# Performance work log

Measured on AMD Instinct MI355X. Metric: run time of the kernel, lower is better.

The kernel has to match this reference:

```python
import jax, jax.numpy as jnp
import numpy as np

N_NODES = 50000
BN_EPS = 1e-5


def gcn_conv(x, W, b, src, dst, n):
    # PyG GCNConv: add self-loops, symmetric normalization, linear then scatter-add, bias after.
    h = x @ W                                             # [N, out]
    loops = jnp.arange(n, dtype=src.dtype)
    s = jnp.concatenate([src, loops])                     # [E+N]
    d = jnp.concatenate([dst, loops])                     # [E+N]
    deg = jax.ops.segment_sum(jnp.ones_like(d, dtype=h.dtype), d, num_segments=n)
    dinv = jnp.where(deg > 0, jax.lax.rsqrt(deg), 0.0)    # deg^-1/2
    norm = dinv[s] * dinv[d]                              # [E+N]
    msg = h[s] * norm[:, None]                            # gather + scale
    out = jax.ops.segment_sum(msg, d, num_segments=n)     # scatter-add to targets
    return out + b


def batch_norm(x, gamma, beta):
    # training-mode BatchNorm1d: batch stats over node dim, biased variance
    mean = jnp.mean(x, axis=0)
    var = jnp.mean(jnp.square(x - mean), axis=0)
    return (x - mean) * jax.lax.rsqrt(var + BN_EPS) * gamma + beta


def setup_inputs() -> dict:
    key = jax.random.key(0)
    ks = jax.random.split(key, 4)
    n, e = N_NODES, 800000
    c_in, c_hid, c_out = 128, 128, 64
    x = jax.random.normal(ks[0], (n, c_in), dtype=jnp.float32)
    edge_index = jax.random.randint(ks[1], (2, e), 0, n, dtype=jnp.int64)
    W1 = jax.random.normal(ks[2], (c_in, c_hid), dtype=jnp.float32) / np.sqrt(c_in)
    W2 = jax.random.normal(ks[3], (c_hid, c_out), dtype=jnp.float32) / np.sqrt(c_hid)
    return {
        "x": x,
        "edge_index": edge_index,
        "W1": W1,
        "b1": jnp.zeros((c_hid,), jnp.float32),
        "gamma": jnp.ones((c_hid,), jnp.float32),
        "beta": jnp.zeros((c_hid,), jnp.float32),
        "W2": W2,
        "b2": jnp.zeros((c_out,), jnp.float32),
    }


def reference(x, edge_index, W1, b1, gamma, beta, W2, b2):
    src, dst = edge_index[0], edge_index[1]
    n = x.shape[0]
    h = gcn_conv(x, W1, b1, src, dst, n)
    h = batch_norm(h, gamma, beta)
    h = jax.nn.elu(h)
    z = gcn_conv(h, W2, b2, src, dst, n)
    return z
```

## Files before the change

### kernel.cpp

```cpp
#include <hip/hip_runtime.h>
#include <math.h>

#define C_IN 128
#define C_HID 128
#define C_OUT 64
#define BN_EPS 1e-5f
#define CHUNK 1024
#define NBB 96
#define CAP 108192

typedef unsigned int uint;
typedef int iv4 __attribute__((ext_vector_type(4)));

__device__ __forceinline__ void fma4(float4& a, float s, const float4& b) {
    a.x += s * b.x; a.y += s * b.y; a.z += s * b.z; a.w += s * b.w;
}
__device__ __forceinline__ uint bfr(float f) {
    uint u = __float_as_uint(f);
    return (u + 0x7fffu + ((u >> 16) & 1u)) >> 16;
}
__device__ __forceinline__ uint pk(float a, float b) { return bfr(a) | (bfr(b) << 16); }
__device__ __forceinline__ float bl(uint u) { return __uint_as_float(u << 16); }
__device__ __forceinline__ float bh(uint u) { return __uint_as_float(u & 0xffff0000u); }

__global__ __launch_bounds__(256) void k_zero(int* __restrict__ deg,
                                              float* __restrict__ gsum,
                                              float* __restrict__ gss,
                                              int* __restrict__ bcur, int n) {
    int i = blockIdx.x * 256 + threadIdx.x;
    if (i < n) deg[i] = 0;
    else if (i < n + 128) gsum[i - n] = 0.f;
    else if (i < n + 256) gss[i - n - 128] = 0.f;
    else if (i < n + 264) bcur[i - n - 256] = 0;
}

__global__ __launch_bounds__(256) void k_bucket(const int* __restrict__ src,
                                                const int* __restrict__ dst,
                                                int* __restrict__ deg,
                                                int* __restrict__ bcur,
                                                int2* __restrict__ stage,
                                                int E, float binv) {
    __shared__ int cnt[8], base[8], off[8];
    if (threadIdx.x < 8) { cnt[threadIdx.x] = 0; off[threadIdx.x] = 0; }
    __syncthreads();
    int e0 = blockIdx.x * CHUNK;
    int e1 = e0 + CHUNK; if (e1 > E) e1 = E;
    int nv = (e1 - e0) & ~3;
    for (int e = e0 + threadIdx.x * 4; e < e0 + nv; e += 1024) {
        iv4 d4 = *(const iv4*)&dst[e];
        #pragma unroll
        for (int j = 0; j < 4; ++j) {
            int d = d4[j];
            atomicAdd(&deg[d], 1);
            int b = (int)((float)d * binv); if (b > 7) b = 7;
            atomicAdd(&cnt[b], 1);
        }
    }
    for (int e = e0 + nv + threadIdx.x; e < e1; e += 256) {
        int d = dst[e];
        atomicAdd(&deg[d], 1);
        int b = (int)((float)d * binv); if (b > 7) b = 7;
        atomicAdd(&cnt[b], 1);
    }
    __syncthreads();
    if (threadIdx.x < 8) base[threadIdx.x] = atomicAdd(&bcur[threadIdx.x], cnt[threadIdx.x]);
    __syncthreads();
    for (int e = e0 + threadIdx.x * 4; e < e0 + nv; e += 1024) {
        iv4 d4 = *(const iv4*)&dst[e];
        iv4 s4 = *(const iv4*)&src[e];
        #pragma unroll
        for (int j = 0; j < 4; ++j) {
            int d = d4[j], s = s4[j];
            int b = (int)((float)d * binv); if (b > 7) b = 7;
            int o = base[b] + atomicAdd(&off[b], 1);
            if (o < CAP) stage[(size_t)b * CAP + o] = make_int2(d, s);
        }
    }
    for (int e = e0 + nv + threadIdx.x; e < e1; e += 256) {
        int d = dst[e], s = src[e];
        int b = (int)((float)d * binv); if (b > 7) b = 7;
        int o = base[b] + atomicAdd(&off[b], 1);
        if (o < CAP) stage[(size_t)b * CAP + o] = make_int2(d, s);
    }
}

__global__ __launch_bounds__(256) void k_part(const int* __restrict__ deg,
                                              int* __restrict__ part, int n) {
    int i = blockIdx.x * 256 + threadIdx.x;
    int v = (i < n) ? deg[i] : 0;
    #pragma unroll
    for (int o = 32; o > 0; o >>= 1) v += __shfl_down(v, o);
    __shared__ int ls[4];
    if ((threadIdx.x & 63) == 0) ls[threadIdx.x >> 6] = v;
    __syncthreads();
    if (threadIdx.x == 0) part[blockIdx.x] = ls[0] + ls[1] + ls[2] + ls[3];
}

__global__ __launch_bounds__(256) void k_scanp(int* __restrict__ part, int nb) {
    __shared__ int s[256];
    int tid = threadIdx.x;
    int v = (tid < nb) ? part[tid] : 0;
    s[tid] = v;
    __syncthreads();
    for (int o = 1; o < 256; o <<= 1) {
        int t = (tid >= o) ? s[tid - o] : 0;
        __syncthreads();
        s[tid] += t;
        __syncthreads();
    }
    if (tid < nb) part[tid] = s[tid] - v;
}

__global__ __launch_bounds__(256) void k_apply(const int* __restrict__ deg,
                                               const int* __restrict__ part,
                                               int* __restrict__ rowstart,
                                               int* __restrict__ cursor,
                                               float* __restrict__ dinv, int n) {
    int i = blockIdx.x * 256 + threadIdx.x;
    int d = (i < n) ? deg[i] : 0;
    __shared__ int s[256];
    s[threadIdx.x] = d;
    __syncthreads();
    for (int o = 1; o < 256; o <<= 1) {
        int t = (threadIdx.x >= o) ? s[threadIdx.x - o] : 0;
        __syncthreads();
        s[threadIdx.x] += t;
        __syncthreads();
    }
    int incl = s[threadIdx.x];
    int off = part[blockIdx.x];
    if (i < n) {
        rowstart[i] = off + incl - d;
        cursor[i]   = off + incl - d;
        dinv[i] = rsqrtf((float)(d + 1));
        if (i == n - 1) rowstart[n] = off + incl;
    }
}

__global__ __launch_bounds__(256) void k_fill2(const int2* __restrict__ stage,
                                               const int* __restrict__ bcur,
                                               int* __restrict__ cursor,
                                               int* __restrict__ csr) {
    int b = blockIdx.x & 7;
    int j = blockIdx.x >> 3;
    int cnt = bcur[b]; if (cnt > CAP) cnt = CAP;
    const int2* sp = stage + (size_t)b * CAP;
    for (int i = j * 256 + threadIdx.x; i < cnt; i += NBB * 256) {
        int2 pr = sp[i];
        csr[atomicAdd(&cursor[pr.x], 1)] = pr.y;
    }
}

__global__ __launch_bounds__(256) void k_gemm1(const float* __restrict__ x,
                                               const float* __restrict__ W,
                                               uint* __restrict__ h, int n) {
    __shared__ float xs[64][68];
    __shared__ float ws[64][68];
    const int tid = threadIdx.x;
    const int cg = tid & 15, rg = tid >> 4;
    const int c0 = cg * 4, r0 = rg * 4;
    const int base = blockIdx.x * 64;
    const int ccol = blockIdx.y * 64;

    float4 acc0 = make_float4(0.f, 0.f, 0.f, 0.f);
    float4 acc1 = acc0, acc2 = acc0, acc3 = acc0;

    for (int p = 0; p < 2; ++p) {
        const int k0 = p * 64;
        if (p) __syncthreads();
        for (int idx = tid; idx < 64 * 16; idx += 256) {
            int row = idx >> 4, c4 = (idx & 15) * 4;
            float4 v = make_float4(0.f, 0.f, 0.f, 0.f);
            if (base + row < n) v = *(const float4*)&x[(size_t)(base + row) * C_IN + k0 + c4];
            *(float4*)&xs[row][c4] = v;
        }
        for (int idx = tid; idx < 64 * 16; idx += 256) {
            int kk = idx >> 4, cc = (idx & 15) * 4;
            *(float4*)&ws[kk][cc] = *(const float4*)&W[(size_t)(k0 + kk) * C_HID + ccol + cc];
        }
        __syncthreads();
        for (int kk = 0; kk < 64; kk += 4) {
            float4 xv0 = *(const float4*)&xs[r0 + 0][kk];
            float4 xv1 = *(const float4*)&xs[r0 + 1][kk];
            float4 xv2 = *(const float4*)&xs[r0 + 2][kk];
            float4 xv3 = *(const float4*)&xs[r0 + 3][kk];
            float4 wv0 = *(const float4*)&ws[kk + 0][c0];
            float4 wv1 = *(const float4*)&ws[kk + 1][c0];
            float4 wv2 = *(const float4*)&ws[kk + 2][c0];
            float4 wv3 = *(const float4*)&ws[kk + 3][c0];
            fma4(acc0, xv0.x, wv0); fma4(acc0, xv0.y, wv1); fma4(acc0, xv0.z, wv2); fma4(acc0, xv0.w, wv3);
            fma4(acc1, xv1.x, wv0); fma4(acc1, xv1.y, wv1); fma4(acc1, xv1.z, wv2); fma4(acc1, xv1.w, wv3);
            fma4(acc2, xv2.x, wv0); fma4(acc2, xv2.y, wv1); fma4(acc2, xv2.z, wv2); fma4(acc2, xv2.w, wv3);
            fma4(acc3, xv3.x, wv0); fma4(acc3, xv3.y, wv1); fma4(acc3, xv3.z, wv2); fma4(acc3, xv3.w, wv3);
        }
    }
    const int cu = (ccol + c0) >> 1;
    if (base + r0 + 0 < n) { uint2 o = make_uint2(pk(acc0.x, acc0.y), pk(acc0.z, acc0.w)); *(uint2*)&h[(size_t)(base + r0 + 0) * 64 + cu] = o; }
    if (base + r0 + 1 < n) { uint2 o = make_uint2(pk(acc1.x, acc1.y), pk(acc1.z, acc1.w)); *(uint2*)&h[(size_t)(base + r0 + 1) * 64 + cu] = o; }
    if (base + r0 + 2 < n) { uint2 o = make_uint2(pk(acc2.x, acc2.y), pk(acc2.z, acc2.w)); *(uint2*)&h[(size_t)(base + r0 + 2) * 64 + cu] = o; }
    if (base + r0 + 3 < n) { uint2 o = make_uint2(pk(acc3.x, acc3.y), pk(acc3.z, acc3.w)); *(uint2*)&h[(size_t)(base + r0 + 3) * 64 + cu] = o; }
}

__global__ __launch_bounds__(256) void k_gather1(const uint4* __restrict__ h,
                                                 const float* __restrict__ dinv,
                                                 const int* __restrict__ rowstart,
                                                 const int* __restrict__ csr,
                                                 const float* __restrict__ b,
                                                 uint4* __restrict__ g1, int n) {
    int v = (blockIdx.x * 256 + threadIdx.x) >> 4;
    int l = threadIdx.x & 15;
    if (v >= n) return;
    float dv = dinv[v];
    int s0 = rowstart[v], s1 = rowstart[v + 1];
    float4 aA, aB;
    {
        uint4 u = h[(size_t)v * 16 + l];
        aA.x = dv * bl(u.x); aA.y = dv * bh(u.x); aA.z = dv * bl(u.y); aA.w = dv * bh(u.y);
        aB.x = dv * bl(u.z); aB.y = dv * bh(u.z); aB.z = dv * bl(u.w); aB.w = dv * bh(u.w);
    }
    int e = s0;
    for (; e + 3 < s1; e += 4) {
        int i0 = csr[e], i1 = csr[e + 1], i2 = csr[e + 2], i3 = csr[e + 3];
        float w0 = dinv[i0], w1 = dinv[i1], w2 = dinv[i2], w3 = dinv[i3];
        uint4 u0 = h[(size_t)i0 * 16 + l];
        uint4 u1 = h[(size_t)i1 * 16 + l];
        uint4 u2 = h[(size_t)i2 * 16 + l];
        uint4 u3 = h[(size_t)i3 * 16 + l];
        aA.x += w0 * bl(u0.x) + w1 * bl(u1.x) + w2 * bl(u2.x) + w3 * bl(u3.x);
        aA.y += w0 * bh(u0.x) + w1 * bh(u1.x) + w2 * bh(u2.x) + w3 * bh(u3.x);
        aA.z += w0 * bl(u0.y) + w1 * bl(u1.y) + w2 * bl(u2.y) + w3 * bl(u3.y);
        aA.w += w0 * bh(u0.y) + w1 * bh(u1.y) + w2 * bh(u2.y) + w3 * bh(u3.y);
        aB.x += w0 * bl(u0.z) + w1 * bl(u1.z) + w2 * bl(u2.z) + w3 * bl(u3.z);
        aB.y += w0 * bh(u0.z) + w1 * bh(u1.z) + w2 * bh(u2.z) + w3 * bh(u3.z);
        aB.z += w0 * bl(u0.w) + w1 * bl(u1.w) + w2 * bl(u2.w) + w3 * bl(u3.w);
        aB.w += w0 * bh(u0.w) + w1 * bh(u1.w) + w2 * bh(u2.w) + w3 * bh(u3.w);
    }
    for (; e < s1; ++e) {
        int s = csr[e];
        float w = dinv[s];
        uint4 u = h[(size_t)s * 16 + l];
        aA.x += w * bl(u.x); aA.y += w * bh(u.x); aA.z += w * bl(u.y); aA.w += w * bh(u.y);
        aB.x += w * bl(u.z); aB.y += w * bh(u.z); aB.z += w * bl(u.w); aB.w += w * bh(u.w);
    }
    float4 b0 = *(const float4*)&b[l * 8];
    float4 b1v = *(const float4*)&b[l * 8 + 4];
    uint4 o;
    o.x = pk(aA.x * dv + b0.x,  aA.y * dv + b0.y);
    o.y = pk(aA.z * dv + b0.z,  aA.w * dv + b0.w);
    o.z = pk(aB.x * dv + b1v.x, aB.y * dv + b1v.y);
    o.w = pk(aB.z * dv + b1v.z, aB.w * dv + b1v.w);
    g1[(size_t)v * 16 + l] = o;
}

__global__ __launch_bounds__(256) void k_bnstats(const uint4* __restrict__ g,
                                                 float* __restrict__ gsum,
                                                 float* __restrict__ gss, int n) {
    float4 sA = make_float4(0.f,0.f,0.f,0.f), sB = sA, qA = sA, qB = sA;
    int total = n * 16;
    int stride = gridDim.x * 256;
    for (int i = blockIdx.x * 256 + threadIdx.x; i < total; i += stride) {
        uint4 u = g[i];
        float v0 = bl(u.x), v1 = bh(u.x), v2 = bl(u.y), v3 = bh(u.y);
        float v4 = bl(u.z), v5 = bh(u.z), v6 = bl(u.w), v7 = bh(u.w);
        sA.x += v0; sA.y += v1; sA.z += v2; sA.w += v3;
        sB.x += v4; sB.y += v5; sB.z += v6; sB.w += v7;
        qA.x += v0*v0; qA.y += v1*v1; qA.z += v2*v2; qA.w += v3*v3;
        qB.x += v4*v4; qB.y += v5*v5; qB.z += v6*v6; qB.w += v7*v7;
    }
    __shared__ float sb[128], qb[128];
    if (threadIdx.x < 128) { sb[threadIdx.x] = 0.f; qb[threadIdx.x] = 0.f; }
    __syncthreads();
    int c0 = (threadIdx.x & 15) * 8;
    atomicAdd(&sb[c0+0], sA.x); atomicAdd(&sb[c0+1], sA.y); atomicAdd(&sb[c0+2], sA.z); atomicAdd(&sb[c0+3], sA.w);
    atomicAdd(&sb[c0+4], sB.x); atomicAdd(&sb[c0+5], sB.y); atomicAdd(&sb[c0+6], sB.z); atomicAdd(&sb[c0+7], sB.w);
    atomicAdd(&qb[c0+0], qA.x); atomicAdd(&qb[c0+1], qA.y); atomicAdd(&qb[c0+2], qA.z); atomicAdd(&qb[c0+3], qA.w);
    atomicAdd(&qb[c0+4], qB.x); atomicAdd(&qb[c0+5], qB.y); atomicAdd(&qb[c0+6], qB.z); atomicAdd(&qb[c0+7], qB.w);
    __syncthreads();
    if (threadIdx.x < 128) {
        atomicAdd(&gsum[threadIdx.x], sb[threadIdx.x]);
        atomicAdd(&gss[threadIdx.x], qb[threadIdx.x]);
    }
}

__global__ __launch_bounds__(256) void k_gemm2(const uint4* __restrict__ g1,
                                               const float* __restrict__ W2,
                                               const float* __restrict__ gsum,
                                               const float* __restrict__ gss,
                                               const float* __restrict__ gamma,
                                               const float* __restrict__ beta,
                                               uint* __restrict__ h2, int n) {
    __shared__ float xs[64][68];
    __shared__ float ws[64][68];
    __shared__ float sc[C_HID], sh[C_HID];
    const int tid = threadIdx.x;
    const int cg = tid & 15, rg = tid >> 4;
    const int c0 = cg * 4, r0 = rg * 4;
    const int base = blockIdx.x * 64;

    if (tid < C_HID) {
        float inv_n = 1.f / (float)n;
        float mean = gsum[tid] * inv_n;
        float var = gss[tid] * inv_n - mean * mean;
        float s = gamma[tid] * rsqrtf(var + BN_EPS);
        sc[tid] = s;
        sh[tid] = beta[tid] - mean * s;
    }
    __syncthreads();

    float4 acc0 = make_float4(0.f, 0.f, 0.f, 0.f);
    float4 acc1 = acc0, acc2 = acc0, acc3 = acc0;

    for (int p = 0; p < 2; ++p) {
        const int k0 = p * 64;
        if (p) __syncthreads();
        for (int idx = tid; idx < 64 * 8; idx += 256) {
            int row = idx >> 3, q4 = idx & 7;
            int k = k0 + q4 * 8;
            float4 vA = make_float4(0.f,0.f,0.f,0.f), vB = vA;
            if (base + row < n) {
                uint4 u = g1[(size_t)(base + row) * 16 + (k >> 3)];
                float t;
                t = bl(u.x) * sc[k+0] + sh[k+0]; vA.x = t > 0.f ? t : expm1f(t);
                t = bh(u.x) * sc[k+1] + sh[k+1]; vA.y = t > 0.f ? t : expm1f(t);
                t = bl(u.y) * sc[k+2] + sh[k+2]; vA.z = t > 0.f ? t : expm1f(t);
                t = bh(u.y) * sc[k+3] + sh[k+3]; vA.w = t > 0.f ? t : expm1f(t);
                t = bl(u.z) * sc[k+4] + sh[k+4]; vB.x = t > 0.f ? t : expm1f(t);
                t = bh(u.z) * sc[k+5] + sh[k+5]; vB.y = t > 0.f ? t : expm1f(t);
                t = bl(u.w) * sc[k+6] + sh[k+6]; vB.z = t > 0.f ? t : expm1f(t);
                t = bh(u.w) * sc[k+7] + sh[k+7]; vB.w = t > 0.f ? t : expm1f(t);
            }
            *(float4*)&xs[row][q4 * 8] = vA;
            *(float4*)&xs[row][q4 * 8 + 4] = vB;
        }
        for (int idx = tid; idx < 64 * 16; idx += 256) {
            int kk = idx >> 4, cc = (idx & 15) * 4;
            *(float4*)&ws[kk][cc] = *(const float4*)&W2[(size_t)(k0 + kk) * C_OUT + cc];
        }
        __syncthreads();
        for (int kk = 0; kk < 64; kk += 4) {
            float4 xv0 = *(const float4*)&xs[r0 + 0][kk];
            float4 xv1 = *(const float4*)&xs[r0 + 1][kk];
            float4 xv2 = *(const float4*)&xs[r0 + 2][kk];
            float4 xv3 = *(const float4*)&xs[r0 + 3][kk];
            float4 wv0 = *(const float4*)&ws[kk + 0][c0];
            float4 wv1 = *(const float4*)&ws[kk + 1][c0];
            float4 wv2 = *(const float4*)&ws[kk + 2][c0];
            float4 wv3 = *(const float4*)&ws[kk + 3][c0];
            fma4(acc0, xv0.x, wv0); fma4(acc0, xv0.y, wv1); fma4(acc0, xv0.z, wv2); fma4(acc0, xv0.w, wv3);
            fma4(acc1, xv1.x, wv0); fma4(acc1, xv1.y, wv1); fma4(acc1, xv1.z, wv2); fma4(acc1, xv1.w, wv3);
            fma4(acc2, xv2.x, wv0); fma4(acc2, xv2.y, wv1); fma4(acc2, xv2.z, wv2); fma4(acc2, xv2.w, wv3);
            fma4(acc3, xv3.x, wv0); fma4(acc3, xv3.y, wv1); fma4(acc3, xv3.z, wv2); fma4(acc3, xv3.w, wv3);
        }
    }
    const int cu = c0 >> 1;
    if (base + r0 + 0 < n) { uint2 o = make_uint2(pk(acc0.x, acc0.y), pk(acc0.z, acc0.w)); *(uint2*)&h2[(size_t)(base + r0 + 0) * 32 + cu] = o; }
    if (base + r0 + 1 < n) { uint2 o = make_uint2(pk(acc1.x, acc1.y), pk(acc1.z, acc1.w)); *(uint2*)&h2[(size_t)(base + r0 + 1) * 32 + cu] = o; }
    if (base + r0 + 2 < n) { uint2 o = make_uint2(pk(acc2.x, acc2.y), pk(acc2.z, acc2.w)); *(uint2*)&h2[(size_t)(base + r0 + 2) * 32 + cu] = o; }
    if (base + r0 + 3 < n) { uint2 o = make_uint2(pk(acc3.x, acc3.y), pk(acc3.z, acc3.w)); *(uint2*)&h2[(size_t)(base + r0 + 3) * 32 + cu] = o; }
}

__global__ __launch_bounds__(256) void k_gather2(const uint2* __restrict__ h,
                                                 const float* __restrict__ dinv,
                                                 const int* __restrict__ rowstart,
                                                 const int* __restrict__ csr,
                                                 const float* __restrict__ b,
                                                 float* __restrict__ out, int n) {
    int v = (blockIdx.x * 256 + threadIdx.x) >> 4;
    int l = threadIdx.x & 15;
    if (v >= n) return;
    float dv = dinv[v];
    int s0 = rowstart[v], s1 = rowstart[v + 1];
    float4 a;
    {
        uint2 u = h[(size_t)v * 16 + l];
        a.x = dv * bl(u.x); a.y = dv * bh(u.x); a.z = dv * bl(u.y); a.w = dv * bh(u.y);
    }
    int e = s0;
    for (; e + 3 < s1; e += 4) {
        int i0 = csr[e], i1 = csr[e + 1], i2 = csr[e + 2], i3 = csr[e + 3];
        float w0 = dinv[i0], w1 = dinv[i1], w2 = dinv[i2], w3 = dinv[i3];
        uint2 u0 = h[(size_t)i0 * 16 + l];
        uint2 u1 = h[(size_t)i1 * 16 + l];
        uint2 u2 = h[(size_t)i2 * 16 + l];
        uint2 u3 = h[(size_t)i3 * 16 + l];
        a.x += w0 * bl(u0.x) + w1 * bl(u1.x) + w2 * bl(u2.x) + w3 * bl(u3.x);
        a.y += w0 * bh(u0.x) + w1 * bh(u1.x) + w2 * bh(u2.x) + w3 * bh(u3.x);
        a.z += w0 * bl(u0.y) + w1 * bl(u1.y) + w2 * bl(u2.y) + w3 * bl(u3.y);
        a.w += w0 * bh(u0.y) + w1 * bh(u1.y) + w2 * bh(u2.y) + w3 * bh(u3.y);
    }
    for (; e < s1; ++e) {
        int s = csr[e];
        float w = dinv[s];
        uint2 u = h[(size_t)s * 16 + l];
        a.x += w * bl(u.x); a.y += w * bh(u.x); a.z += w * bl(u.y); a.w += w * bh(u.y);
    }
    float4 bb = *(const float4*)&b[l * 4];
    float4 o;
    o.x = a.x * dv + bb.x; o.y = a.y * dv + bb.y;
    o.z = a.z * dv + bb.z; o.w = a.w * dv + bb.w;
    *(float4*)&out[(size_t)v * C_OUT + l * 4] = o;
}

extern "C" void kernel_launch(void* const* d_in, const int* in_sizes, int n_in,
                              void* d_out, int out_size, void* d_ws, size_t ws_size,
                              hipStream_t stream) {
    const float* x     = (const float*)d_in[0];
    const int*   ei    = (const int*)d_in[1];
    const float* W1    = (const float*)d_in[2];
    const float* b1    = (const float*)d_in[3];
    const float* gamma = (const float*)d_in[4];
    const float* beta  = (const float*)d_in[5];
    const float* W2    = (const float*)d_in[6];
    const float* b2    = (const float*)d_in[7];
    float* out = (float*)d_out;

    const int n = in_sizes[0] / C_IN;
    const int E = in_sizes[1] / 2;
    const int* src = ei;
    const int* dst = ei + E;

    char* p = (char*)d_ws;
    auto carve = [&](size_t bytes) {
        char* r = p;
        p += (bytes + 255) & ~(size_t)255;
        return r;
    };
    int*   deg      = (int*)  carve((size_t)n * 4);
    int*   rowstart = (int*)  carve((size_t)(n + 1) * 4);
    int*   cursor   = (int*)  carve((size_t)n * 4);
    int*   csr      = (int*)  carve((size_t)E * 4);
    float* dinv     = (float*)carve((size_t)n * 4);
    uint*  h1       = (uint*) carve((size_t)n * 64 * 4);
    uint*  g1       = (uint*) carve((size_t)n * 64 * 4);
    uint*  h2       = (uint*) carve((size_t)n * 32 * 4);
    float* gsum     = (float*)carve(C_HID * 4);
    float* gss      = (float*)carve(C_HID * 4);
    int*   part     = (int*)  carve(256 * 4);
    int*   bcur     = (int*)  carve(8 * 4);
    int2*  stage    = (int2*) carve((size_t)8 * CAP * 8);

    const int nb = (n + 255) / 256;
    const int gblocks = (n * 16 + 255) / 256;
    const int fc = (E + CHUNK - 1) / CHUNK;
    const float binv = 8.0f / (float)n;

    k_zero<<<(n + 264 + 255) / 256, 256, 0, stream>>>(deg, gsum, gss, bcur, n);
    k_bucket<<<fc, 256, 0, stream>>>(src, dst, deg, bcur, stage, E, binv);
    k_gemm1<<<dim3((n + 63) / 64, 2), 256, 0, stream>>>(x, W1, h1, n);
    k_part<<<nb, 256, 0, stream>>>(deg, part, n);
    k_scanp<<<1, 256, 0, stream>>>(part, nb);
    k_apply<<<nb, 256, 0, stream>>>(deg, part, rowstart, cursor, dinv, n);
    k_fill2<<<8 * NBB, 256, 0, stream>>>(stage, bcur, cursor, csr);
    k_gather1<<<gblocks, 256, 0, stream>>>((const uint4*)h1, dinv, rowstart, csr, b1, (uint4*)g1, n);
    k_bnstats<<<512, 256, 0, stream>>>((const uint4*)g1, gsum, gss, n);
    k_gemm2<<<(n + 63) / 64, 256, 0, stream>>>((const uint4*)g1, W2, gsum, gss, gamma, beta, h2, n);
    k_gather2<<<gblocks, 256, 0, stream>>>((const uint2*)h2, dinv, rowstart, csr, b2, out, n);
}
```

Measured before the change: 217.3 us.

## Use bf16 MFMA for both dense GEMMs instead of scalar FP32 FMAs

Both node-feature GEMMs are rewritten to stage bf16-packed inputs and transposed weights in LDS and compute with the 16x16x32 bf16 matrix-core instruction. GEMM1 now covers all 128 output columns in one block instead of splitting across two grid columns. Inputs are rounded to bf16 before multiplication, which adds precision loss compared with FP32 FMA. Output stores become scattered 16-bit writes instead of packed 64-bit writes.

```diff
diff --git a/kernel.cpp b/kernel.cpp
--- a/kernel.cpp
+++ b/kernel.cpp
@@ -8,13 +8,14 @@
 #define CHUNK 1024
 #define NBB 96
 #define CAP 108192
+#define LSTR 67
 
 typedef unsigned int uint;
+typedef unsigned short ushort;
 typedef int iv4 __attribute__((ext_vector_type(4)));
-
-__device__ __forceinline__ void fma4(float4& a, float s, const float4& b) {
-    a.x += s * b.x; a.y += s * b.y; a.z += s * b.z; a.w += s * b.w;
-}
+typedef short bfx8 __attribute__((ext_vector_type(8)));
+typedef float fx4 __attribute__((ext_vector_type(4)));
+
 __device__ __forceinline__ uint bfr(float f) {
     uint u = __float_as_uint(f);
     return (u + 0x7fffu + ((u >> 16) & 1u)) >> 16;
@@ -153,52 +154,62 @@
 
 __global__ __launch_bounds__(256) void k_gemm1(const float* __restrict__ x,
                                                const float* __restrict__ W,
-                                               uint* __restrict__ h, int n) {
-    __shared__ float xs[64][68];
-    __shared__ float ws[64][68];
+                                               ushort* __restrict__ h, int n) {
+    __shared__ uint xsp[64 * LSTR];
+    __shared__ uint wtp[128 * LSTR];
     const int tid = threadIdx.x;
-    const int cg = tid & 15, rg = tid >> 4;
-    const int c0 = cg * 4, r0 = rg * 4;
+    const int w = tid >> 6, l = tid & 63;
+    const int lo = l & 15, hi = l >> 4;
     const int base = blockIdx.x * 64;
-    const int ccol = blockIdx.y * 64;
-
-    float4 acc0 = make_float4(0.f, 0.f, 0.f, 0.f);
-    float4 acc1 = acc0, acc2 = acc0, acc3 = acc0;
-
-    for (int p = 0; p < 2; ++p) {
-        const int k0 = p * 64;
-        if (p) __syncthreads();
-        for (int idx = tid; idx < 64 * 16; idx += 256) {
-            int row = idx >> 4, c4 = (idx & 15) * 4;
-            float4 v = make_float4(0.f, 0.f, 0.f, 0.f);
-            if (base + row < n) v = *(const float4*)&x[(size_t)(base + row) * C_IN + k0 + c4];
-            *(float4*)&xs[row][c4] = v;
-        }
-        for (int idx = tid; idx < 64 * 16; idx += 256) {
-            int kk = idx >> 4, cc = (idx & 15) * 4;
-            *(float4*)&ws[kk][cc] = *(const float4*)&W[(size_t)(k0 + kk) * C_HID + ccol + cc];
-        }
-        __syncthreads();
-        for (int kk = 0; kk < 64; kk += 4) {
-            float4 xv0 = *(const float4*)&xs[r0 + 0][kk];
-            float4 xv1 = *(const float4*)&xs[r0 + 1][kk];
-            float4 xv2 = *(const float4*)&xs[r0 + 2][kk];
-            float4 xv3 = *(const float4*)&xs[r0 + 3][kk];
-            float4 wv0 = *(const float4*)&ws[kk + 0][c0];
-            float4 wv1 = *(const float4*)&ws[kk + 1][c0];
-            float4 wv2 = *(const float4*)&ws[kk + 2][c0];
-            float4 wv3 = *(const float4*)&ws[kk + 3][c0];
-            fma4(acc0, xv0.x, wv0); fma4(acc0, xv0.y, wv1); fma4(acc0, xv0.z, wv2); fma4(acc0, xv0.w, wv3);
-            fma4(acc1, xv1.x, wv0); fma4(acc1, xv1.y, wv1); fma4(acc1, xv1.z, wv2); fma4(acc1, xv1.w, wv3);
-            fma4(acc2, xv2.x, wv0); fma4(acc2, xv2.y, wv1); fma4(acc2, xv2.z, wv2); fma4(acc2, xv2.w, wv3);
-            fma4(acc3, xv3.x, wv0); fma4(acc3, xv3.y, wv1); fma4(acc3, xv3.z, wv2); fma4(acc3, xv3.w, wv3);
-        }
-    }
-    const int cu = (ccol + c0) >> 1;
-    if (base + r0 + 0 < n) { uint2 o = make_uint2(pk(acc0.x, acc0.y), pk(acc0.z, acc0.w)); *(uint2*)&h[(size_t)(base + r0 + 0) * 64 + cu] = o; }
-    if (base + r0 + 1 < n) { uint2 o = make_uint2(pk(acc1.x, acc1.y), pk(acc1.z, acc1.w)); *(uint2*)&h[(size_t)(base + r0 + 1) * 64 + cu] = o; }
-    if (base + r0 + 2 < n) { uint2 o = make_uint2(pk(acc2.x, acc2.y), pk(acc2.z, acc2.w)); *(uint2*)&h[(size_t)(base + r0 + 2) * 64 + cu] = o; }
-    if (base + r0 + 3 < n) { uint2 o = make_uint2(pk(acc3.x, acc3.y), pk(acc3.z, acc3.w)); *(uint2*)&h[(size_t)(base + r0 + 3) * 64 + cu] = o; }
+
+    for (int idx = tid; idx < 64 * 32; idx += 256) {
+        int row = idx >> 5, c4 = (idx & 31) * 4;
+        float4 v = make_float4(0.f, 0.f, 0.f, 0.f);
+        if (base + row < n) v = *(const float4*)&x[(size_t)(base + row) * C_IN + c4];
+        xsp[row * LSTR + (c4 >> 1)]     = pk(v.x, v.y);
+        xsp[row * LSTR + (c4 >> 1) + 1] = pk(v.z, v.w);
+    }
+    for (int idx = tid; idx < 64 * 32; idx += 256) {
+        int kk = idx >> 5, n4 = (idx & 31) * 4;
+        float4 w0 = *(const float4*)&W[(size_t)(2 * kk) * C_HID + n4];
+        float4 w1 = *(const float4*)&W[(size_t)(2 * kk + 1) * C_HID + n4];
+        wtp[(n4 + 0) * LSTR + kk] = pk(w0.x, w1.x);
+        wtp[(n4 + 1) * LSTR + kk] = pk(w0.y, w1.y);
+        wtp[(n4 + 2) * LSTR + kk] = pk(w0.z, w1.z);
+        wtp[(n4 + 3) * LSTR + kk] = pk(w0.w, w1.w);
+    }
+    __syncthreads();
+
+    fx4 acc[8];
+    #pragma unroll
+    for (int t = 0; t < 8; ++t) acc[t] = (fx4)(0.f);
+
+    const int arow = (w * 16 + lo) * LSTR;
+    #pragma unroll
+    for (int kb = 0; kb < 4; ++kb) {
+        const int ka = kb * 16 + hi * 4;
+        uint4 ua;
+        ua.x = xsp[arow + ka]; ua.y = xsp[arow + ka + 1];
+        ua.z = xsp[arow + ka + 2]; ua.w = xsp[arow + ka + 3];
+        bfx8 af = __builtin_bit_cast(bfx8, ua);
+        #pragma unroll
+        for (int nt = 0; nt < 8; ++nt) {
+            const int brow = (nt * 16 + lo) * LSTR;
+            uint4 ub;
+            ub.x = wtp[brow + ka]; ub.y = wtp[brow + ka + 1];
+            ub.z = wtp[brow + ka + 2]; ub.w = wtp[brow + ka + 3];
+            bfx8 bf_ = __builtin_bit_cast(bfx8, ub);
+            acc[nt] = __builtin_amdgcn_mfma_f32_16x16x32_bf16(af, bf_, acc[nt], 0, 0, 0);
+        }
+    }
+    #pragma unroll
+    for (int nt = 0; nt < 8; ++nt) {
+        #pragma unroll
+        for (int r = 0; r < 4; ++r) {
+            int row = base + w * 16 + hi * 4 + r;
+            if (row < n) h[(size_t)row * C_HID + nt * 16 + lo] = (ushort)bfr(acc[nt][r]);
+        }
+    }
 }
 
 __global__ __launch_bounds__(256) void k_gather1(const uint4* __restrict__ h,
@@ -288,13 +299,13 @@
                                                const float* __restrict__ gss,
                                                const float* __restrict__ gamma,
                                                const float* __restrict__ beta,
-                                               uint* __restrict__ h2, int n) {
-    __shared__ float xs[64][68];
-    __shared__ float ws[64][68];
+                                               ushort* __restrict__ h2, int n) {
+    __shared__ uint xsp[64 * LSTR];
+    __shared__ uint wtp[64 * LSTR];
     __shared__ float sc[C_HID], sh[C_HID];
     const int tid = threadIdx.x;
-    const int cg = tid & 15, rg = tid >> 4;
-    const int c0 = cg * 4, r0 = rg * 4;
+    const int w = tid >> 6, l = tid & 63;
+    const int lo = l & 15, hi = l >> 4;
     const int base = blockIdx.x * 64;
 
     if (tid < C_HID) {
@@ -307,56 +318,68 @@
     }
     __syncthreads();
 
-    float4 acc0 = make_float4(0.f, 0.f, 0.f, 0.f);
-    float4 acc1 = acc0, acc2 = acc0, acc3 = acc0;
-
-    for (int p = 0; p < 2; ++p) {
-        const int k0 = p * 64;
-        if (p) __syncthreads();
-        for (int idx = tid; idx < 64 * 8; idx += 256) {
-            int row = idx >> 3, q4 = idx & 7;
-            int k = k0 + q4 * 8;
-            float4 vA = make_float4(0.f,0.f,0.f,0.f), vB = vA;
-            if (base + row < n) {
-                uint4 u = g1[(size_t)(base + row) * 16 + (k >> 3)];
-                float t;
-                t = bl(u.x) * sc[k+0] + sh[k+0]; vA.x = t > 0.f ? t : expm1f(t);
-                t = bh(u.x) * sc[k+1] + sh[k+1]; vA.y = t > 0.f ? t : expm1f(t);
-                t = bl(u.y) * sc[k+2] + sh[k+2]; vA.z = t > 0.f ? t : expm1f(t);
-                t = bh(u.y) * sc[k+3] + sh[k+3]; vA.w = t > 0.f ? t : expm1f(t);
-                t = bl(u.z) * sc[k+4] + sh[k+4]; vB.x = t > 0.f ? t : expm1f(t);
-                t = bh(u.z) * sc[k+5] + sh[k+5]; vB.y = t > 0.f ? t : expm1f(t);
-                t = bl(u.w) * sc[k+6] + sh[k+6]; vB.z = t > 0.f ? t : expm1f(t);
-                t = bh(u.w) * sc[k+7] + sh[k+7]; vB.w = t > 0.f ? t : expm1f(t);
-            }
-            *(float4*)&xs[row][q4 * 8] = vA;
-            *(float4*)&xs[row][q4 * 8 + 4] = vB;
-        }
-        for (int idx = tid; idx < 64 * 16; idx += 256) {
-            int kk = idx >> 4, cc = (idx & 15) * 4;
-            *(float4*)&ws[kk][cc] = *(const float4*)&W2[(size_t)(k0 + kk) * C_OUT + cc];
-        }
-        __syncthreads();
-        for (int kk = 0; kk < 64; kk += 4) {
-            float4 xv0 = *(const float4*)&xs[r0 + 0][kk];
-            float4 xv1 = *(const float4*)&xs[r0 + 1][kk];
-            float4 xv2 = *(const float4*)&xs[r0 + 2][kk];
-            float4 xv3 = *(const float4*)&xs[r0 + 3][kk];
-            float4 wv0 = *(const float4*)&ws[kk + 0][c0];
-            float4 wv1 = *(const float4*)&ws[kk + 1][c0];
-            float4 wv2 = *(const float4*)&ws[kk + 2][c0];
-            float4 wv3 = *(const float4*)&ws[kk + 3][c0];
-            fma4(acc0, xv0.x, wv0); fma4(acc0, xv0.y, wv1); fma4(acc0, xv0.z, wv2); fma4(acc0, xv0.w, wv3);
-            fma4(acc1, xv1.x, wv0); fma4(acc1, xv1.y, wv1); fma4(acc1, xv1.z, wv2); fma4(acc1, xv1.w, wv3);
-            fma4(acc2, xv2.x, wv0); fma4(acc2, xv2.y, wv1); fma4(acc2, xv2.z, wv2); fma4(acc2, xv2.w, wv3);
-            fma4(acc3, xv3.x, wv0); fma4(acc3, xv3.y, wv1); fma4(acc3, xv3.z, wv2); fma4(acc3, xv3.w, wv3);
-        }
-    }
-    const int cu = c0 >> 1;
-    if (base + r0 + 0 < n) { uint2 o = make_uint2(pk(acc0.x, acc0.y), pk(acc0.z, acc0.w)); *(uint2*)&h2[(size_t)(base + r0 + 0) * 32 + cu] = o; }
-    if (base + r0 + 1 < n) { uint2 o = make_uint2(pk(acc1.x, acc1.y), pk(acc1.z, acc1.w)); *(uint2*)&h2[(size_t)(base + r0 + 1) * 32 + cu] = o; }
-    if (base + r0 + 2 < n) { uint2 o = make_uint2(pk(acc2.x, acc2.y), pk(acc2.z, acc2.w)); *(uint2*)&h2[(size_t)(base + r0 + 2) * 32 + cu] = o; }
-    if (base + r0 + 3 < n) { uint2 o = make_uint2(pk(acc3.x, acc3.y), pk(acc3.z, acc3.w)); *(uint2*)&h2[(size_t)(base + r0 + 3) * 32 + cu] = o; }
+    for (int idx = tid; idx < 64 * 16; idx += 256) {
+        int row = idx >> 4, q = idx & 15;
+        int k8 = q * 8;
+        uint4 u = make_uint4(0, 0, 0, 0);
+        if (base + row < n) u = g1[(size_t)(base + row) * 16 + q];
+        float t;
+        float e0, e1, e2, e3, e4, e5, e6, e7;
+        t = bl(u.x) * sc[k8+0] + sh[k8+0]; e0 = t > 0.f ? t : expm1f(t);
+        t = bh(u.x) * sc[k8+1] + sh[k8+1]; e1 = t > 0.f ? t : expm1f(t);
+        t = bl(u.y) * sc[k8+2] + sh[k8+2]; e2 = t > 0.f ? t : expm1f(t);
+        t = bh(u.y) * sc[k8+3] + sh[k8+3]; e3 = t > 0.f ? t : expm1f(t);
+        t = bl(u.z) * sc[k8+4] + sh[k8+4]; e4 = t > 0.f ? t : expm1f(t);
+        t = bh(u.z) * sc[k8+5] + sh[k8+5]; e5 = t > 0.f ? t : expm1f(t);
+        t = bl(u.w) * sc[k8+6] + sh[k8+6]; e6 = t > 0.f ? t : expm1f(t);
+        t = bh(u.w) * sc[k8+7] + sh[k8+7]; e7 = t > 0.f ? t : expm1f(t);
+        int wbase = row * LSTR + q * 4;
+        xsp[wbase + 0] = pk(e0, e1);
+        xsp[wbase + 1] = pk(e2, e3);
+        xsp[wbase + 2] = pk(e4, e5);
+        xsp[wbase + 3] = pk(e6, e7);
+    }
+    for (int idx = tid; idx < 64 * 16; idx += 256) {
+        int kk = idx >> 4, n4 = (idx & 15) * 4;
+        float4 w0 = *(const float4*)&W2[(size_t)(2 * kk) * C_OUT + n4];
+        float4 w1 = *(const float4*)&W2[(size_t)(2 * kk + 1) * C_OUT + n4];
+        wtp[(n4 + 0) * LSTR + kk] = pk(w0.x, w1.x);
+        wtp[(n4 + 1) * LSTR + kk] = pk(w0.y, w1.y);
+        wtp[(n4 + 2) * LSTR + kk] = pk(w0.z, w1.z);
+        wtp[(n4 + 3) * LSTR + kk] = pk(w0.w, w1.w);
+    }
+    __syncthreads();
+
+    fx4 acc[4];
+    #pragma unroll
+    for (int t = 0; t < 4; ++t) acc[t] = (fx4)(0.f);
+
+    const int arow = (w * 16 + lo) * LSTR;
+    #pragma unroll
+    for (int kb = 0; kb < 4; ++kb) {
+        const int ka = kb * 16 + hi * 4;
+        uint4 ua;
+        ua.x = xsp[arow + ka]; ua.y = xsp[arow + ka + 1];
+        ua.z = xsp[arow + ka + 2]; ua.w = xsp[arow + ka + 3];
+        bfx8 af = __builtin_bit_cast(bfx8, ua);
+        #pragma unroll
+        for (int nt = 0; nt < 4; ++nt) {
+            const int brow = (nt * 16 + lo) * LSTR;
+            uint4 ub;
+            ub.x = wtp[brow + ka]; ub.y = wtp[brow + ka + 1];
+            ub.z = wtp[brow + ka + 2]; ub.w = wtp[brow + ka + 3];
+            bfx8 bf_ = __builtin_bit_cast(bfx8, ub);
+            acc[nt] = __builtin_amdgcn_mfma_f32_16x16x32_bf16(af, bf_, acc[nt], 0, 0, 0);
+        }
+    }
+    #pragma unroll
+    for (int nt = 0; nt < 4; ++nt) {
+        #pragma unroll
+        for (int r = 0; r < 4; ++r) {
+            int row = base + w * 16 + hi * 4 + r;
+            if (row < n) h2[(size_t)row * C_OUT + nt * 16 + lo] = (ushort)bfr(acc[nt][r]);
+        }
+    }
 }
 
 __global__ __launch_bounds__(256) void k_gather2(const uint2* __restrict__ h,
@@ -425,19 +448,19 @@
         p += (bytes + 255) & ~(size_t)255;
         return r;
     };
-    int*   deg      = (int*)  carve((size_t)n * 4);
-    int*   rowstart = (int*)  carve((size_t)(n + 1) * 4);
-    int*   cursor   = (int*)  carve((size_t)n * 4);
-    int*   csr      = (int*)  carve((size_t)E * 4);
-    float* dinv     = (float*)carve((size_t)n * 4);
-    uint*  h1       = (uint*) carve((size_t)n * 64 * 4);
-    uint*  g1       = (uint*) carve((size_t)n * 64 * 4);
-    uint*  h2       = (uint*) carve((size_t)n * 32 * 4);
-    float* gsum     = (float*)carve(C_HID * 4);
-    float* gss      = (float*)carve(C_HID * 4);
-    int*   part     = (int*)  carve(256 * 4);
-    int*   bcur     = (int*)  carve(8 * 4);
-    int2*  stage    = (int2*) carve((size_t)8 * CAP * 8);
+    int*    deg      = (int*)   carve((size_t)n * 4);
+    int*    rowstart = (int*)   carve((size_t)(n + 1) * 4);
+    int*    cursor   = (int*)   carve((size_t)n * 4);
+    int*    csr      = (int*)   carve((size_t)E * 4);
+    float*  dinv     = (float*) carve((size_t)n * 4);
+    ushort* h1       = (ushort*)carve((size_t)n * 128 * 2);
+    ushort* g1       = (ushort*)carve((size_t)n * 128 * 2);
+    ushort* h2       = (ushort*)carve((size_t)n * 64 * 2);
+    float*  gsum     = (float*) carve(C_HID * 4);
+    float*  gss      = (float*) carve(C_HID * 4);
+    int*    part     = (int*)   carve(256 * 4);
+    int*    bcur     = (int*)   carve(8 * 4);
+    int2*   stage    = (int2*)  carve((size_t)8 * CAP * 8);
 
     const int nb = (n + 255) / 256;
     const int gblocks = (n * 16 + 255) / 256;
@@ -446,7 +469,7 @@
 
     k_zero<<<(n + 264 + 255) / 256, 256, 0, stream>>>(deg, gsum, gss, bcur, n);
     k_bucket<<<fc, 256, 0, stream>>>(src, dst, deg, bcur, stage, E, binv);
-    k_gemm1<<<dim3((n + 63) / 64, 2), 256, 0, stream>>>(x, W1, h1, n);
+    k_gemm1<<<(n + 63) / 64, 256, 0, stream>>>(x, W1, h1, n);
     k_part<<<nb, 256, 0, stream>>>(deg, part, n);
     k_scanp<<<1, 256, 0, stream>>>(part, nb);
     k_apply<<<nb, 256, 0, stream>>>(deg, part, rowstart, cursor, dinv, n);
```

Measured after the change: 192.3 us. 11.5% less time.
